# Kernel tuning notes

Measured on AMD Instinct MI355X. Metric: run time of the kernel, lower is better.

Reference implementation:

```python
import jax, jax.numpy as jnp
import numpy as np

IN_SIZE = 64
RES = 1024
B = 16
T = 2048
ALPHA = 0.5
SPECTRAL_RADIUS = 0.9


def setup_inputs() -> dict:
    key = jax.random.key(0)
    ks = jax.random.split(key, 8)
    # W_hh scaled so spectral radius ~ SPECTRAL_RADIUS (circular law: |eig|max ~ sqrt(R)*std)
    scale_hh = SPECTRAL_RADIUS / np.sqrt(RES)
    return {
        "x": jax.random.normal(ks[0], (B, T, IN_SIZE), dtype=jnp.float32),
        "W_in0": jax.random.normal(ks[1], (IN_SIZE, RES), dtype=jnp.float32) * 0.5,
        "W_hh0": jax.random.normal(ks[2], (RES, RES), dtype=jnp.float32) * scale_hh,
        "b0": jax.random.normal(ks[3], (1, RES), dtype=jnp.float32) * 0.5,
        "W_in1": jax.random.normal(ks[4], (RES, RES), dtype=jnp.float32) * 0.1,
        "W_hh1": jax.random.normal(ks[5], (RES, RES), dtype=jnp.float32) * scale_hh,
        "b1": jax.random.normal(ks[6], (1, RES), dtype=jnp.float32) * 0.5,
        "readout": jax.random.normal(ks[7], (2 * RES, IN_SIZE), dtype=jnp.float32) * 0.02,
    }


def _reservoir_layer(xs, W_in, W_hh, b, alpha):
    # xs: [T, B, F] time-major; sequential leaky-integrator scan over T
    h0 = jnp.zeros((xs.shape[1], W_hh.shape[0]), dtype=xs.dtype)

    def step(h, x_i):
        h = (1.0 - alpha) * h + alpha * jnp.tanh(x_i @ W_in + h @ W_hh + b)
        return h, h

    _, states = jax.lax.scan(step, h0, xs)
    return states  # [T, B, R]


def reference(x, W_in0, W_hh0, b0, W_in1, W_hh1, b1, readout):
    xt = jnp.transpose(x, (1, 0, 2))  # [T, B, in]
    s0 = _reservoir_layer(xt, W_in0, W_hh0, b0, ALPHA)  # [T, B, R]
    s1 = _reservoir_layer(s0, W_in1, W_hh1, b1, ALPHA)  # [T, B, R]
    h = jnp.concatenate([s0, s1], axis=-1)  # [T, B, 2R]
    out = h @ readout  # [T, B, in]
    return jnp.transpose(out, (1, 0, 2))  # [B, T, in]
```

## Files before the change

kernel.cpp:

```cpp
#include <hip/hip_runtime.h>
#include <math.h>

#define ESN_B 16
#define ESN_T 2048
#define ESN_R 1024
#define ESN_IN 64
#define NBR (ESN_B * ESN_R)

#define OFF_WT_HH0 0
#define OFF_WT_IN1 (1024 * 1024)
#define OFF_WT_HH1 (2 * 1024 * 1024)
#define OFF_WT_IN0 (3 * 1024 * 1024)
#define OFF_RT     (OFF_WT_IN0 + 1024 * 64)
#define OFF_S0G    (OFF_RT + 64 * 2048)
#define OFF_S1G    (OFF_S0G + 2 * NBR)
#define OFF_FLAGS  (OFF_S1G + 2 * NBR)

typedef float vfloat4 __attribute__((__vector_size__(16)));

__global__ void __launch_bounds__(256) transpose_k(const float* __restrict__ src,
                                                   float* __restrict__ dst,
                                                   int rows, int cols) {
  __shared__ float tile[32][33];
  int bx = blockIdx.x * 32, by = blockIdx.y * 32;
  int tx = threadIdx.x, ty = threadIdx.y;
  #pragma unroll
  for (int i = ty; i < 32; i += 8) {
    int r = by + i, c = bx + tx;
    if (r < rows && c < cols) tile[i][tx] = src[(size_t)r * cols + c];
  }
  __syncthreads();
  #pragma unroll
  for (int i = ty; i < 32; i += 8) {
    int c = bx + i, r = by + tx;
    if (c < cols && r < rows) dst[(size_t)c * rows + r] = tile[tx][i];
  }
}

__device__ __forceinline__ float fast_tanh(float v) {
  float a = fabsf(v);
  float e = __expf(-2.0f * a);
  float t = __fdividef(1.0f - e, 1.0f + e);
  return copysignf(t, v);
}

__device__ __forceinline__ float dot4(float4 a, float4 b, float acc) {
  acc = fmaf(a.x, b.x, acc);
  acc = fmaf(a.y, b.y, acc);
  acc = fmaf(a.z, b.z, acc);
  acc = fmaf(a.w, b.w, acc);
  return acc;
}

__device__ __forceinline__ float wave_red64(float v) {
  #pragma unroll
  for (int off = 32; off > 0; off >>= 1) v += __shfl_xor(v, off, 64);
  return v;
}

__device__ __forceinline__ float reduce2(float a0, float a1, bool lb0) {
  float u = lb0 ? a0 : a1, k = lb0 ? a1 : a0;
  float A = k + __shfl_xor(u, 1, 64);
  A += __shfl_xor(A, 2, 64);
  A += __shfl_xor(A, 4, 64);
  A += __shfl_xor(A, 8, 64);
  A += __shfl_xor(A, 16, 64);
  A += __shfl_xor(A, 32, 64);
  return A;
}

__device__ __forceinline__ void llc_store_f32x4(float* p, float4 v) {
  vfloat4 vv = {v.x, v.y, v.z, v.w};
  asm volatile("global_store_dwordx4 %0, %1, off sc1" :: "v"(p), "v"(vv) : "memory");
}
__device__ __forceinline__ void llc_store_u32(unsigned* p, unsigned v) {
  asm volatile("global_store_dword %0, %1, off sc1" :: "v"(p), "v"(v) : "memory");
}
__device__ __forceinline__ unsigned llc_load_u32(const unsigned* p) {
  unsigned f;
  asm volatile("global_load_dword %0, %1, off sc1\n\ts_waitcnt vmcnt(0)"
               : "=v"(f) : "v"(p) : "memory");
  return f;
}
__device__ __forceinline__ void vmcnt0() {
  asm volatile("s_waitcnt vmcnt(0)" ::: "memory");
}
__device__ __forceinline__ void barrier_only() {
  asm volatile("" ::: "memory");
  __builtin_amdgcn_s_barrier();
  asm volatile("" ::: "memory");
}
__device__ __forceinline__ void barrier_lgkm() {
  asm volatile("s_waitcnt lgkmcnt(0)" ::: "memory");
  __builtin_amdgcn_s_barrier();
  asm volatile("" ::: "memory");
}

__global__ void __launch_bounds__(512, 2) esn_scan_kernel(
    const float* __restrict__ x,
    const float* __restrict__ b0,
    const float* __restrict__ b1,
    float* __restrict__ wsf,
    float* __restrict__ out) {
  __shared__ float s0l[2][4][1024];
  __shared__ float s1l[4][1024];
  __shared__ __align__(16) float res[2][4][16];
  extern __shared__ float dyn_pad[];
  if (blockIdx.x == 0x7fffffffu) dyn_pad[0] = 1.0f;

  const float* wtHH0 = wsf + OFF_WT_HH0;
  const float* wtIN1 = wsf + OFF_WT_IN1;
  const float* wtHH1 = wsf + OFF_WT_HH1;
  const float* wtIN0 = wsf + OFF_WT_IN0;
  const float* rt    = wsf + OFF_RT;
  float* s0g = wsf + OFF_S0G;
  float* s1g = wsf + OFF_S1G;
  unsigned* flags = (unsigned*)(wsf + OFF_FLAGS);

  const int tid = threadIdx.x;
  const int l = tid & 63;
  const int w = tid >> 6;
  const int bid = blockIdx.x;
  const int g = bid >> 6;
  const int bg = bid & 63;
  const int batch0 = g * 4;
  const int wg = bg * 8 + w;
  const int c0 = wg * 2;
  const int wl2 = w * 2;
  const bool doRO = (w >= 4);
  const int rbl = w - 4;
  const int rb = batch0 + rbl;
  const int roc = bg;
  unsigned* gflags = flags + g * 64;
  const bool lb0 = (l & 1) != 0;

  float4 wA0_0, wA0_1, wA0_2, wA0_3, wA1_0, wA1_1, wA1_2, wA1_3;
  float4 wB0_0, wB0_1, wB0_2, wB0_3, wB1_0, wB1_1, wB1_2, wB1_3;
  float4 wC0_0, wC0_1, wC0_2, wC0_3, wC1_0, wC1_1, wC1_2, wC1_3;
  float4 rd0, rd1, rd2, rd3, rd4, rd5, rd6, rd7;

#define LOADW(cc) { \
    const float* pA = wtHH0 + (size_t)(c0 + cc) * ESN_R + l * 4; \
    const float* pB = wtIN1 + (size_t)(c0 + cc) * ESN_R + l * 4; \
    const float* pC = wtHH1 + (size_t)(c0 + cc) * ESN_R + l * 4; \
    wA##cc##_0 = *(const float4*)(pA);       wA##cc##_1 = *(const float4*)(pA + 256); \
    wA##cc##_2 = *(const float4*)(pA + 512); wA##cc##_3 = *(const float4*)(pA + 768); \
    wB##cc##_0 = *(const float4*)(pB);       wB##cc##_1 = *(const float4*)(pB + 256); \
    wB##cc##_2 = *(const float4*)(pB + 512); wB##cc##_3 = *(const float4*)(pB + 768); \
    wC##cc##_0 = *(const float4*)(pC);       wC##cc##_1 = *(const float4*)(pC + 256); \
    wC##cc##_2 = *(const float4*)(pC + 512); wC##cc##_3 = *(const float4*)(pC + 768); \
  }
  LOADW(0) LOADW(1)
#undef LOADW

  rd0 = rd1 = rd2 = rd3 = rd4 = rd5 = rd6 = rd7 = make_float4(0.f, 0.f, 0.f, 0.f);
  if (doRO) {
    const float* pr = rt + (size_t)roc * 2048 + l * 4;
    rd0 = *(const float4*)(pr);        rd1 = *(const float4*)(pr + 256);
    rd2 = *(const float4*)(pr + 512);  rd3 = *(const float4*)(pr + 768);
    rd4 = *(const float4*)(pr + 1024); rd5 = *(const float4*)(pr + 1280);
    rd6 = *(const float4*)(pr + 1536); rd7 = *(const float4*)(pr + 1792);
  }
  const float wI0 = wtIN0[(size_t)(c0 + 0) * ESN_IN + l];
  const float wI1 = wtIN0[(size_t)(c0 + 1) * ESN_IN + l];
  const float b0sel = b0[c0 + (l & 1)];
  const float b1sel = b1[c0 + (l & 1)];

  const float* sA0 = s0g + 0 * NBR + batch0 * ESN_R + tid * 4;
  const float* sA1 = s0g + 1 * NBR + batch0 * ESN_R + tid * 4;
  const float* sB0 = s1g + 0 * NBR + batch0 * ESN_R + tid * 4;
  const float* sB1 = s1g + 1 * NBR + batch0 * ESN_R + tid * 4;
  const int soff = (l >> 2) * ESN_R + (l & 3) * 4;
  float* st0A = s0g + 0 * NBR + batch0 * ESN_R + bg * 16 + soff;
  float* st0B = s0g + 1 * NBR + batch0 * ESN_R + bg * 16 + soff;
  float* st1A = s1g + 0 * NBR + batch0 * ESN_R + bg * 16 + soff;
  float* st1B = s1g + 1 * NBR + batch0 * ESN_R + bg * 16 + soff;
  const float* xbase = x + (size_t)batch0 * ESN_T * ESN_IN + l;

#define ESN_ROUND(SLOTC, rr)                                                   \
  {                                                                            \
    const bool doL0 = ((rr) < ESN_T);                                          \
    const bool doL1 = ((rr) >= 1 && (rr) <= ESN_T);                            \
    float xv0 = 0.f, xv1 = 0.f, xv2 = 0.f, xv3 = 0.f;                          \
    if (doL0) {                                                                \
      const float* xp = xbase + (size_t)(rr) * ESN_IN;                         \
      xv0 = xp[0 * ESN_T * ESN_IN];                                            \
      xv1 = xp[1 * ESN_T * ESN_IN];                                            \
      xv2 = xp[2 * ESN_T * ESN_IN];                                            \
      xv3 = xp[3 * ESN_T * ESN_IN];                                            \
    }                                                                          \
    vmcnt0();                                                                  \
    if ((rr) > 0) {                                                            \
      if (w == 0) {                                                            \
        while (!__all(llc_load_u32(&gflags[l]) >= (unsigned)(rr))) {}          \
      }                                                                        \
      barrier_only();                                               \
    }                                                                          \
    const float* p0 = SLOTC ? sA0 : sA1;        \
    const float* p1 = SLOTC ? sB0 : sB1;                                       \
    float4 t0, t1, u0, u1;                                                     \
    asm volatile(                                                              \
        "global_load_dwordx4 %0, %4, off sc1\n\t"                              \
        "global_load_dwordx4 %1, %5, off sc1\n\t"                              \
        "global_load_dwordx4 %2, %6, off sc1\n\t"                              \
        "global_load_dwordx4 %3, %7, off sc1\n\t"                              \
        "s_waitcnt vmcnt(2)"                                                   \
        : "=&v"(t0), "=&v"(t1), "=&v"(u0), "=&v"(u1)                           \
        : "v"(p0), "v"(p0 + 2048), "v"(p1), "v"(p1 + 2048)                     \
        : "memory");                                                           \
    {                                                                          \
      float* d0 = &s0l[SLOTC][0][0] + tid * 4;                                 \
      *(float4*)(d0)        = t0;                                              \
      *(float4*)(d0 + 2048) = t1;                                              \
    }                                                                          \
    barrier_lgkm();                  \
    if (doL0) {                                                                \
      _Pragma("unroll")                                                        \
      for (int bb = 0; bb < 4; ++bb) {                                         \
        const float* hp = &s0l[SLOTC][bb][l * 4];                              \
        float4 h0x = *(const float4*)(hp);                                     \
        float4 h1x = *(const float4*)(hp + 256);                               \
        float4 h2x = *(const float4*)(hp + 512);                               \
        float4 h3x = *(const float4*)(hp + 768);                               \
        float xb = (bb == 0) ? xv0 : (bb == 1) ? xv1 : (bb == 2) ? xv2 : xv3;  \
        float a0 = xb * wI0, a1 = xb * wI1;                                    \
        a0 = dot4(wA0_0, h0x, a0); a0 = dot4(wA0_1, h1x, a0);                  \
        a0 = dot4(wA0_2, h2x, a0); a0 = dot4(wA0_3, h3x, a0);                  \
        a1 = dot4(wA1_0, h0x, a1); a1 = dot4(wA1_1, h1x, a1);                  \
        a1 = dot4(wA1_2, h2x, a1); a1 = dot4(wA1_3, h3x, a1);                  \
        float C = reduce2(a0, a1, lb0);                                        \
        if (l < 2) {                                                           \
          float prev = s0l[SLOTC][bb][c0 + l];                                 \
          res[0][bb][wl2 + l] = 0.5f * prev + 0.5f * fast_tanh(C + b0sel);     \
        }                                                                      \
      }                                                                        \
    }                                                                          \
    vmcnt0();                                                                  \
    {                                                                          \
      float* d1 = &s1l[0][0] + tid * 4;                                        \
      *(float4*)(d1)        = u0;                                              \
      *(float4*)(d1 + 2048) = u1;                                              \
    }                                                                          \
    barrier_lgkm();                             \
    if (w == 0 && l < 16 && doL0) {                                            \
      float4 v0 = *(const float4*)&res[0][l >> 2][(l & 3) * 4];                \
      llc_store_f32x4(SLOTC ? st0B : st0A, v0);                                \
    }                                                                          \
    if (doL1) {                                                                \
      _Pragma("unroll")                                                        \
      for (int bb = 0; bb < 4; ++bb) {                                         \
        const float* hp = &s0l[SLOTC][bb][l * 4];                              \
        float4 h0x = *(const float4*)(hp);                                     \
        float4 h1x = *(const float4*)(hp + 256);                               \
        float4 h2x = *(const float4*)(hp + 512);                               \
        float4 h3x = *(const float4*)(hp + 768);                               \
        const float* gp = &s1l[bb][l * 4];                                     \
        float4 g0x = *(const float4*)(gp);                                     \
        float4 g1x = *(const float4*)(gp + 256);                               \
        float4 g2x = *(const float4*)(gp + 512);                               \
        float4 g3x = *(const float4*)(gp + 768);                               \
        float a0 = 0.f, a1 = 0.f;                                              \
        a0 = dot4(wB0_0, h0x, a0); a0 = dot4(wB0_1, h1x, a0);                  \
        a0 = dot4(wB0_2, h2x, a0); a0 = dot4(wB0_3, h3x, a0);                  \
        a0 = dot4(wC0_0, g0x, a0); a0 = dot4(wC0_1, g1x, a0);                  \
        a0 = dot4(wC0_2, g2x, a0); a0 = dot4(wC0_3, g3x, a0);                  \
        a1 = dot4(wB1_0, h0x, a1); a1 = dot4(wB1_1, h1x, a1);                  \
        a1 = dot4(wB1_2, h2x, a1); a1 = dot4(wB1_3, h3x, a1);                  \
        a1 = dot4(wC1_0, g0x, a1); a1 = dot4(wC1_1, g1x, a1);                  \
        a1 = dot4(wC1_2, g2x, a1); a1 = dot4(wC1_3, g3x, a1);                  \
        float C = reduce2(a0, a1, lb0);                                        \
        if (l < 2) {                                                           \
          float prev = s1l[bb][c0 + l];                                        \
          res[1][bb][wl2 + l] = 0.5f * prev + 0.5f * fast_tanh(C + b1sel);     \
        }                                                                      \
      }                                                                        \
    }                                                                          \
    barrier_lgkm();                                   \
    if (w == 0) {                                                              \
      if (l < 16 && doL1) {                                                    \
        float4 v1 = *(const float4*)&res[1][l >> 2][(l & 3) * 4];              \
        llc_store_f32x4(SLOTC ? st1B : st1A, v1);                              \
      }                                                                        \
      vmcnt0();                                                                \
      if (l == 0) llc_store_u32(&gflags[bg], (unsigned)((rr) + 1));            \
    }                                                                          \
    if ((rr) >= 2 && doRO) {                                                   \
      const float* sp = &s0l[1 - SLOTC][rbl][l * 4];                           \
      const float* tp = &s1l[rbl][l * 4];                                      \
      float a = 0.f;                                                           \
      a = dot4(rd0, *(const float4*)(sp), a);                                  \
      a = dot4(rd1, *(const float4*)(sp + 256), a);                            \
      a = dot4(rd2, *(const float4*)(sp + 512), a);                            \
      a = dot4(rd3, *(const float4*)(sp + 768), a);                            \
      a = dot4(rd4, *(const float4*)(tp), a);                                  \
      a = dot4(rd5, *(const float4*)(tp + 256), a);                            \
      a = dot4(rd6, *(const float4*)(tp + 512), a);                            \
      a = dot4(rd7, *(const float4*)(tp + 768), a);                            \
      a = wave_red64(a);                                                       \
      if (l == 0) out[((size_t)rb * ESN_T + ((rr) - 2)) * ESN_IN + roc] = a;   \
    }                                                                          \
  }

  for (int rp = 0; rp < (ESN_T + 2) / 2; ++rp) {
    const int r0 = rp * 2;
    ESN_ROUND(0, r0)
    ESN_ROUND(1, r0 + 1)
  }
#undef ESN_ROUND
}

extern "C" void kernel_launch(void* const* d_in, const int* in_sizes, int n_in,
                              void* d_out, int out_size, void* d_ws, size_t ws_size,
                              hipStream_t stream) {
  (void)in_sizes; (void)n_in; (void)out_size; (void)ws_size;
  const float* x     = (const float*)d_in[0];
  const float* w_in0 = (const float*)d_in[1];
  const float* w_hh0 = (const float*)d_in[2];
  const float* b0    = (const float*)d_in[3];
  const float* w_in1 = (const float*)d_in[4];
  const float* w_hh1 = (const float*)d_in[5];
  const float* b1    = (const float*)d_in[6];
  const float* rdo   = (const float*)d_in[7];
  float* out = (float*)d_out;
  float* wsf = (float*)d_ws;

  dim3 tb(32, 8);
  transpose_k<<<dim3(32, 32), tb, 0, stream>>>(w_hh0, wsf + OFF_WT_HH0, 1024, 1024);
  transpose_k<<<dim3(32, 32), tb, 0, stream>>>(w_in1, wsf + OFF_WT_IN1, 1024, 1024);
  transpose_k<<<dim3(32, 32), tb, 0, stream>>>(w_hh1, wsf + OFF_WT_HH1, 1024, 1024);
  transpose_k<<<dim3(32, 2),  tb, 0, stream>>>(w_in0, wsf + OFF_WT_IN0, 64, 1024);
  transpose_k<<<dim3(2, 64),  tb, 0, stream>>>(rdo,   wsf + OFF_RT, 2048, 64);

  (void)hipMemsetAsync(wsf + OFF_S0G + NBR, 0, NBR * sizeof(float), stream);
  (void)hipMemsetAsync(wsf + OFF_S1G, 0, NBR * sizeof(float), stream);
  (void)hipMemsetAsync(wsf + OFF_FLAGS, 0, 4 * 64 * sizeof(unsigned), stream);

  esn_scan_kernel<<<dim3(256), dim3(512), 40960, stream>>>(x, b0, b1, wsf, out);
}
```

Baseline: 12.17 ms.

## Use 1024-thread blocks with one output column per wave

Each block now runs 16 waves instead of 8, and each wave owns a single reservoir column rather than two. That halves per-thread weight registers and replaces the paired two-column reduction with a plain 64-lane reduction. Staging the shared state into LDS now takes one float4 per thread instead of two. The trade-off is larger workgroups with a 1-block-per-CU launch bound, and barriers that span more waves.

```diff
diff --git a/kernel.cpp b/kernel.cpp
--- a/kernel.cpp
+++ b/kernel.cpp
@@ -58,17 +58,6 @@
   return v;
 }
 
-__device__ __forceinline__ float reduce2(float a0, float a1, bool lb0) {
-  float u = lb0 ? a0 : a1, k = lb0 ? a1 : a0;
-  float A = k + __shfl_xor(u, 1, 64);
-  A += __shfl_xor(A, 2, 64);
-  A += __shfl_xor(A, 4, 64);
-  A += __shfl_xor(A, 8, 64);
-  A += __shfl_xor(A, 16, 64);
-  A += __shfl_xor(A, 32, 64);
-  return A;
-}
-
 __device__ __forceinline__ void llc_store_f32x4(float* p, float4 v) {
   vfloat4 vv = {v.x, v.y, v.z, v.w};
   asm volatile("global_store_dwordx4 %0, %1, off sc1" :: "v"(p), "v"(vv) : "memory");
@@ -96,7 +85,7 @@
   asm volatile("" ::: "memory");
 }
 
-__global__ void __launch_bounds__(512, 2) esn_scan_kernel(
+__global__ void __launch_bounds__(1024, 1) esn_scan_kernel(
     const float* __restrict__ x,
     const float* __restrict__ b0,
     const float* __restrict__ b1,
@@ -124,35 +113,28 @@
   const int g = bid >> 6;
   const int bg = bid & 63;
   const int batch0 = g * 4;
-  const int wg = bg * 8 + w;
-  const int c0 = wg * 2;
-  const int wl2 = w * 2;
-  const bool doRO = (w >= 4);
-  const int rbl = w - 4;
+  const int c0 = bg * 16 + w;
+  const bool doRO = (w >= 12);
+  const int rbl = w - 12;
   const int rb = batch0 + rbl;
   const int roc = bg;
   unsigned* gflags = flags + g * 64;
-  const bool lb0 = (l & 1) != 0;
-
-  float4 wA0_0, wA0_1, wA0_2, wA0_3, wA1_0, wA1_1, wA1_2, wA1_3;
-  float4 wB0_0, wB0_1, wB0_2, wB0_3, wB1_0, wB1_1, wB1_2, wB1_3;
-  float4 wC0_0, wC0_1, wC0_2, wC0_3, wC1_0, wC1_1, wC1_2, wC1_3;
+
+  float4 wA_0, wA_1, wA_2, wA_3;
+  float4 wB_0, wB_1, wB_2, wB_3;
+  float4 wC_0, wC_1, wC_2, wC_3;
   float4 rd0, rd1, rd2, rd3, rd4, rd5, rd6, rd7;
-
-#define LOADW(cc) { \
-    const float* pA = wtHH0 + (size_t)(c0 + cc) * ESN_R + l * 4; \
-    const float* pB = wtIN1 + (size_t)(c0 + cc) * ESN_R + l * 4; \
-    const float* pC = wtHH1 + (size_t)(c0 + cc) * ESN_R + l * 4; \
-    wA##cc##_0 = *(const float4*)(pA);       wA##cc##_1 = *(const float4*)(pA + 256); \
-    wA##cc##_2 = *(const float4*)(pA + 512); wA##cc##_3 = *(const float4*)(pA + 768); \
-    wB##cc##_0 = *(const float4*)(pB);       wB##cc##_1 = *(const float4*)(pB + 256); \
-    wB##cc##_2 = *(const float4*)(pB + 512); wB##cc##_3 = *(const float4*)(pB + 768); \
-    wC##cc##_0 = *(const float4*)(pC);       wC##cc##_1 = *(const float4*)(pC + 256); \
-    wC##cc##_2 = *(const float4*)(pC + 512); wC##cc##_3 = *(const float4*)(pC + 768); \
-  }
-  LOADW(0) LOADW(1)
-#undef LOADW
-
+  {
+    const float* pA = wtHH0 + (size_t)c0 * ESN_R + l * 4;
+    const float* pB = wtIN1 + (size_t)c0 * ESN_R + l * 4;
+    const float* pC = wtHH1 + (size_t)c0 * ESN_R + l * 4;
+    wA_0 = *(const float4*)(pA);       wA_1 = *(const float4*)(pA + 256);
+    wA_2 = *(const float4*)(pA + 512); wA_3 = *(const float4*)(pA + 768);
+    wB_0 = *(const float4*)(pB);       wB_1 = *(const float4*)(pB + 256);
+    wB_2 = *(const float4*)(pB + 512); wB_3 = *(const float4*)(pB + 768);
+    wC_0 = *(const float4*)(pC);       wC_1 = *(const float4*)(pC + 256);
+    wC_2 = *(const float4*)(pC + 512); wC_3 = *(const float4*)(pC + 768);
+  }
   rd0 = rd1 = rd2 = rd3 = rd4 = rd5 = rd6 = rd7 = make_float4(0.f, 0.f, 0.f, 0.f);
   if (doRO) {
     const float* pr = rt + (size_t)roc * 2048 + l * 4;
@@ -161,10 +143,9 @@
     rd4 = *(const float4*)(pr + 1024); rd5 = *(const float4*)(pr + 1280);
     rd6 = *(const float4*)(pr + 1536); rd7 = *(const float4*)(pr + 1792);
   }
-  const float wI0 = wtIN0[(size_t)(c0 + 0) * ESN_IN + l];
-  const float wI1 = wtIN0[(size_t)(c0 + 1) * ESN_IN + l];
-  const float b0sel = b0[c0 + (l & 1)];
-  const float b1sel = b1[c0 + (l & 1)];
+  const float wI = wtIN0[(size_t)c0 * ESN_IN + l];
+  const float b0sel = b0[c0];
+  const float b1sel = b1[c0];
 
   const float* sA0 = s0g + 0 * NBR + batch0 * ESN_R + tid * 4;
   const float* sA1 = s0g + 1 * NBR + batch0 * ESN_R + tid * 4;
@@ -198,22 +179,16 @@
     }                                                                          \
     const float* p0 = SLOTC ? sA0 : sA1;        \
     const float* p1 = SLOTC ? sB0 : sB1;                                       \
-    float4 t0, t1, u0, u1;                                                     \
+    float4 t0, u0;                                                             \
     asm volatile(                                                              \
-        "global_load_dwordx4 %0, %4, off sc1\n\t"                              \
-        "global_load_dwordx4 %1, %5, off sc1\n\t"                              \
-        "global_load_dwordx4 %2, %6, off sc1\n\t"                              \
-        "global_load_dwordx4 %3, %7, off sc1\n\t"                              \
-        "s_waitcnt vmcnt(2)"                                                   \
-        : "=&v"(t0), "=&v"(t1), "=&v"(u0), "=&v"(u1)                           \
-        : "v"(p0), "v"(p0 + 2048), "v"(p1), "v"(p1 + 2048)                     \
+        "global_load_dwordx4 %0, %2, off sc1\n\t"                              \
+        "global_load_dwordx4 %1, %3, off sc1\n\t"                              \
+        "s_waitcnt vmcnt(1)"                                                   \
+        : "=&v"(t0), "=&v"(u0)                                                 \
+        : "v"(p0), "v"(p1)                                                     \
         : "memory");                                                           \
-    {                                                                          \
-      float* d0 = &s0l[SLOTC][0][0] + tid * 4;                                 \
-      *(float4*)(d0)        = t0;                                              \
-      *(float4*)(d0 + 2048) = t1;                                              \
-    }                                                                          \
-    barrier_lgkm();                  \
+    *(float4*)(&s0l[SLOTC][0][0] + tid * 4) = t0;                              \
+    barrier_lgkm();                   \
     if (doL0) {                                                                \
       _Pragma("unroll")                                                        \
       for (int bb = 0; bb < 4; ++bb) {                                         \
@@ -223,24 +198,18 @@
         float4 h2x = *(const float4*)(hp + 512);                               \
         float4 h3x = *(const float4*)(hp + 768);                               \
         float xb = (bb == 0) ? xv0 : (bb == 1) ? xv1 : (bb == 2) ? xv2 : xv3;  \
-        float a0 = xb * wI0, a1 = xb * wI1;                                    \
-        a0 = dot4(wA0_0, h0x, a0); a0 = dot4(wA0_1, h1x, a0);                  \
-        a0 = dot4(wA0_2, h2x, a0); a0 = dot4(wA0_3, h3x, a0);                  \
-        a1 = dot4(wA1_0, h0x, a1); a1 = dot4(wA1_1, h1x, a1);                  \
-        a1 = dot4(wA1_2, h2x, a1); a1 = dot4(wA1_3, h3x, a1);                  \
-        float C = reduce2(a0, a1, lb0);                                        \
-        if (l < 2) {                                                           \
-          float prev = s0l[SLOTC][bb][c0 + l];                                 \
-          res[0][bb][wl2 + l] = 0.5f * prev + 0.5f * fast_tanh(C + b0sel);     \
+        float a0 = xb * wI;                                                    \
+        a0 = dot4(wA_0, h0x, a0); a0 = dot4(wA_1, h1x, a0);                    \
+        a0 = dot4(wA_2, h2x, a0); a0 = dot4(wA_3, h3x, a0);                    \
+        float C = wave_red64(a0);                                              \
+        if (l == 0) {                                                          \
+          float prev = s0l[SLOTC][bb][c0];                                     \
+          res[0][bb][w] = 0.5f * prev + 0.5f * fast_tanh(C + b0sel);           \
         }                                                                      \
       }                                                                        \
     }                                                                          \
     vmcnt0();                                                                  \
-    {                                                                          \
-      float* d1 = &s1l[0][0] + tid * 4;                                        \
-      *(float4*)(d1)        = u0;                                              \
-      *(float4*)(d1 + 2048) = u1;                                              \
-    }                                                                          \
+    *(float4*)(&s1l[0][0] + tid * 4) = u0;                                     \
     barrier_lgkm();                             \
     if (w == 0 && l < 16 && doL0) {                                            \
       float4 v0 = *(const float4*)&res[0][l >> 2][(l & 3) * 4];                \
@@ -259,19 +228,15 @@
         float4 g1x = *(const float4*)(gp + 256);                               \
         float4 g2x = *(const float4*)(gp + 512);                               \
         float4 g3x = *(const float4*)(gp + 768);                               \
-        float a0 = 0.f, a1 = 0.f;                                              \
-        a0 = dot4(wB0_0, h0x, a0); a0 = dot4(wB0_1, h1x, a0);                  \
-        a0 = dot4(wB0_2, h2x, a0); a0 = dot4(wB0_3, h3x, a0);                  \
-        a0 = dot4(wC0_0, g0x, a0); a0 = dot4(wC0_1, g1x, a0);                  \
-        a0 = dot4(wC0_2, g2x, a0); a0 = dot4(wC0_3, g3x, a0);                  \
-        a1 = dot4(wB1_0, h0x, a1); a1 = dot4(wB1_1, h1x, a1);                  \
-        a1 = dot4(wB1_2, h2x, a1); a1 = dot4(wB1_3, h3x, a1);                  \
-        a1 = dot4(wC1_0, g0x, a1); a1 = dot4(wC1_1, g1x, a1);                  \
-        a1 = dot4(wC1_2, g2x, a1); a1 = dot4(wC1_3, g3x, a1);                  \
-        float C = reduce2(a0, a1, lb0);                                        \
-        if (l < 2) {                                                           \
-          float prev = s1l[bb][c0 + l];                                        \
-          res[1][bb][wl2 + l] = 0.5f * prev + 0.5f * fast_tanh(C + b1sel);     \
+        float a0 = 0.f;                                                        \
+        a0 = dot4(wB_0, h0x, a0); a0 = dot4(wB_1, h1x, a0);                    \
+        a0 = dot4(wB_2, h2x, a0); a0 = dot4(wB_3, h3x, a0);                    \
+        a0 = dot4(wC_0, g0x, a0); a0 = dot4(wC_1, g1x, a0);                    \
+        a0 = dot4(wC_2, g2x, a0); a0 = dot4(wC_3, g3x, a0);                    \
+        float C = wave_red64(a0);                                              \
+        if (l == 0) {                                                          \
+          float prev = s1l[bb][c0];                                            \
+          res[1][bb][w] = 0.5f * prev + 0.5f * fast_tanh(C + b1sel);           \
         }                                                                      \
       }                                                                        \
     }                                                                          \
@@ -335,5 +300,5 @@
   (void)hipMemsetAsync(wsf + OFF_S1G, 0, NBR * sizeof(float), stream);
   (void)hipMemsetAsync(wsf + OFF_FLAGS, 0, 4 * 64 * sizeof(unsigned), stream);
 
-  esn_scan_kernel<<<dim3(256), dim3(512), 40960, stream>>>(x, b0, b1, wsf, out);
-}
+  esn_scan_kernel<<<dim3(256), dim3(1024), 40960, stream>>>(x, b0, b1, wsf, out);
+}
```

New measurement: 18.19 ms. 49.5% more time.

## Merge layer-0 and layer-1 round phases into one pass with joint reduction

Applied to the files above, without the earlier changes.

Fuses the separate layer-0 and layer-1 compute phases of each scan round into a single loop. All four accumulators are reduced in one combined cross-lane shuffle tree, and both layers' states are stored by one wave in a single store phase. This removes one workgroup barrier and one wait-for-memory point per round, shortening the serial critical path of the 2048-step scan. In exchange it waits on all global state loads before any compute, and it raises register pressure from holding more live accumulators and h/g vectors at once.

```diff
diff --git a/kernel.cpp b/kernel.cpp
--- a/kernel.cpp
+++ b/kernel.cpp
@@ -58,15 +58,19 @@
   return v;
 }
 
-__device__ __forceinline__ float reduce2(float a0, float a1, bool lb0) {
-  float u = lb0 ? a0 : a1, k = lb0 ? a1 : a0;
-  float A = k + __shfl_xor(u, 1, 64);
-  A += __shfl_xor(A, 2, 64);
-  A += __shfl_xor(A, 4, 64);
-  A += __shfl_xor(A, 8, 64);
-  A += __shfl_xor(A, 16, 64);
-  A += __shfl_xor(A, 32, 64);
-  return A;
+__device__ __forceinline__ float reduce4(float a0, float a1, float a2, float a3,
+                                         bool lb0, bool lb1) {
+  float uA = lb0 ? a0 : a1, kA = lb0 ? a1 : a0;
+  float A = kA + __shfl_xor(uA, 1, 64);
+  float uB = lb0 ? a2 : a3, kB = lb0 ? a3 : a2;
+  float B = kB + __shfl_xor(uB, 1, 64);
+  float uC = lb1 ? A : B, kC = lb1 ? B : A;
+  float C = kC + __shfl_xor(uC, 2, 64);
+  C += __shfl_xor(C, 4, 64);
+  C += __shfl_xor(C, 8, 64);
+  C += __shfl_xor(C, 16, 64);
+  C += __shfl_xor(C, 32, 64);
+  return C;
 }
 
 __device__ __forceinline__ void llc_store_f32x4(float* p, float4 v) {
@@ -133,6 +137,7 @@
   const int roc = bg;
   unsigned* gflags = flags + g * 64;
   const bool lb0 = (l & 1) != 0;
+  const bool lb1 = (l & 2) != 0;
 
   float4 wA0_0, wA0_1, wA0_2, wA0_3, wA1_0, wA1_1, wA1_2, wA1_3;
   float4 wB0_0, wB0_1, wB0_2, wB0_3, wB1_0, wB1_1, wB1_2, wB1_3;
@@ -163,18 +168,17 @@
   }
   const float wI0 = wtIN0[(size_t)(c0 + 0) * ESN_IN + l];
   const float wI1 = wtIN0[(size_t)(c0 + 1) * ESN_IN + l];
-  const float b0sel = b0[c0 + (l & 1)];
-  const float b1sel = b1[c0 + (l & 1)];
+  float bsel = 0.f;
+  if (l < 4) bsel = ((l < 2) ? b0 : b1)[c0 + (l & 1)];
 
   const float* sA0 = s0g + 0 * NBR + batch0 * ESN_R + tid * 4;
   const float* sA1 = s0g + 1 * NBR + batch0 * ESN_R + tid * 4;
   const float* sB0 = s1g + 0 * NBR + batch0 * ESN_R + tid * 4;
   const float* sB1 = s1g + 1 * NBR + batch0 * ESN_R + tid * 4;
-  const int soff = (l >> 2) * ESN_R + (l & 3) * 4;
-  float* st0A = s0g + 0 * NBR + batch0 * ESN_R + bg * 16 + soff;
-  float* st0B = s0g + 1 * NBR + batch0 * ESN_R + bg * 16 + soff;
-  float* st1A = s1g + 0 * NBR + batch0 * ESN_R + bg * 16 + soff;
-  float* st1B = s1g + 1 * NBR + batch0 * ESN_R + bg * 16 + soff;
+  float* gb = ((l < 16) ? s0g : s1g) +
+              (batch0 + ((l >> 2) & 3)) * ESN_R + bg * 16 + (l & 3) * 4;
+  float* gbA = gb;
+  float* gbB = gb + NBR;
   const float* xbase = x + (size_t)batch0 * ESN_T * ESN_IN + l;
 
 #define ESN_ROUND(SLOTC, rr)                                                   \
@@ -189,12 +193,11 @@
       xv2 = xp[2 * ESN_T * ESN_IN];                                            \
       xv3 = xp[3 * ESN_T * ESN_IN];                                            \
     }                                                                          \
-    vmcnt0();                                                                  \
     if ((rr) > 0) {                                                            \
       if (w == 0) {                                                            \
         while (!__all(llc_load_u32(&gflags[l]) >= (unsigned)(rr))) {}          \
       }                                                                        \
-      barrier_only();                                               \
+      barrier_only();            \
     }                                                                          \
     const float* p0 = SLOTC ? sA0 : sA1;        \
     const float* p1 = SLOTC ? sB0 : sB1;                                       \
@@ -204,82 +207,60 @@
         "global_load_dwordx4 %1, %5, off sc1\n\t"                              \
         "global_load_dwordx4 %2, %6, off sc1\n\t"                              \
         "global_load_dwordx4 %3, %7, off sc1\n\t"                              \
-        "s_waitcnt vmcnt(2)"                                                   \
+        "s_waitcnt vmcnt(0)"                                                   \
         : "=&v"(t0), "=&v"(t1), "=&v"(u0), "=&v"(u1)                           \
         : "v"(p0), "v"(p0 + 2048), "v"(p1), "v"(p1 + 2048)                     \
         : "memory");                                                           \
     {                                                                          \
       float* d0 = &s0l[SLOTC][0][0] + tid * 4;                                 \
+      float* d1 = &s1l[0][0] + tid * 4;                                        \
       *(float4*)(d0)        = t0;                                              \
       *(float4*)(d0 + 2048) = t1;                                              \
-    }                                                                          \
-    barrier_lgkm();                  \
-    if (doL0) {                                                                \
-      _Pragma("unroll")                                                        \
-      for (int bb = 0; bb < 4; ++bb) {                                         \
-        const float* hp = &s0l[SLOTC][bb][l * 4];                              \
-        float4 h0x = *(const float4*)(hp);                                     \
-        float4 h1x = *(const float4*)(hp + 256);                               \
-        float4 h2x = *(const float4*)(hp + 512);                               \
-        float4 h3x = *(const float4*)(hp + 768);                               \
-        float xb = (bb == 0) ? xv0 : (bb == 1) ? xv1 : (bb == 2) ? xv2 : xv3;  \
-        float a0 = xb * wI0, a1 = xb * wI1;                                    \
-        a0 = dot4(wA0_0, h0x, a0); a0 = dot4(wA0_1, h1x, a0);                  \
-        a0 = dot4(wA0_2, h2x, a0); a0 = dot4(wA0_3, h3x, a0);                  \
-        a1 = dot4(wA1_0, h0x, a1); a1 = dot4(wA1_1, h1x, a1);                  \
-        a1 = dot4(wA1_2, h2x, a1); a1 = dot4(wA1_3, h3x, a1);                  \
-        float C = reduce2(a0, a1, lb0);                                        \
-        if (l < 2) {                                                           \
-          float prev = s0l[SLOTC][bb][c0 + l];                                 \
-          res[0][bb][wl2 + l] = 0.5f * prev + 0.5f * fast_tanh(C + b0sel);     \
-        }                                                                      \
-      }                                                                        \
-    }                                                                          \
-    vmcnt0();                                                                  \
-    {                                                                          \
-      float* d1 = &s1l[0][0] + tid * 4;                                        \
       *(float4*)(d1)        = u0;                                              \
       *(float4*)(d1 + 2048) = u1;                                              \
     }                                                                          \
-    barrier_lgkm();                             \
-    if (w == 0 && l < 16 && doL0) {                                            \
-      float4 v0 = *(const float4*)&res[0][l >> 2][(l & 3) * 4];                \
-      llc_store_f32x4(SLOTC ? st0B : st0A, v0);                                \
-    }                                                                          \
-    if (doL1) {                                                                \
-      _Pragma("unroll")                                                        \
-      for (int bb = 0; bb < 4; ++bb) {                                         \
-        const float* hp = &s0l[SLOTC][bb][l * 4];                              \
-        float4 h0x = *(const float4*)(hp);                                     \
-        float4 h1x = *(const float4*)(hp + 256);                               \
-        float4 h2x = *(const float4*)(hp + 512);                               \
-        float4 h3x = *(const float4*)(hp + 768);                               \
-        const float* gp = &s1l[bb][l * 4];                                     \
-        float4 g0x = *(const float4*)(gp);                                     \
-        float4 g1x = *(const float4*)(gp + 256);                               \
-        float4 g2x = *(const float4*)(gp + 512);                               \
-        float4 g3x = *(const float4*)(gp + 768);                               \
-        float a0 = 0.f, a1 = 0.f;                                              \
-        a0 = dot4(wB0_0, h0x, a0); a0 = dot4(wB0_1, h1x, a0);                  \
-        a0 = dot4(wB0_2, h2x, a0); a0 = dot4(wB0_3, h3x, a0);                  \
-        a0 = dot4(wC0_0, g0x, a0); a0 = dot4(wC0_1, g1x, a0);                  \
-        a0 = dot4(wC0_2, g2x, a0); a0 = dot4(wC0_3, g3x, a0);                  \
-        a1 = dot4(wB1_0, h0x, a1); a1 = dot4(wB1_1, h1x, a1);                  \
-        a1 = dot4(wB1_2, h2x, a1); a1 = dot4(wB1_3, h3x, a1);                  \
-        a1 = dot4(wC1_0, g0x, a1); a1 = dot4(wC1_1, g1x, a1);                  \
-        a1 = dot4(wC1_2, g2x, a1); a1 = dot4(wC1_3, g3x, a1);                  \
-        float C = reduce2(a0, a1, lb0);                                        \
-        if (l < 2) {                                                           \
-          float prev = s1l[bb][c0 + l];                                        \
-          res[1][bb][wl2 + l] = 0.5f * prev + 0.5f * fast_tanh(C + b1sel);     \
-        }                                                                      \
+    barrier_lgkm();                                \
+    _Pragma("unroll")                                                          \
+    for (int bb = 0; bb < 4; ++bb) {                                           \
+      const float* hp = &s0l[SLOTC][bb][l * 4];                                \
+      float4 h0x = *(const float4*)(hp);                                       \
+      float4 h1x = *(const float4*)(hp + 256);                                 \
+      float4 h2x = *(const float4*)(hp + 512);                                 \
+      float4 h3x = *(const float4*)(hp + 768);                                 \
+      const float* gp = &s1l[bb][l * 4];                                       \
+      float4 g0x = *(const float4*)(gp);                                       \
+      float4 g1x = *(const float4*)(gp + 256);                                 \
+      float4 g2x = *(const float4*)(gp + 512);                                 \
+      float4 g3x = *(const float4*)(gp + 768);                                 \
+      float xb = (bb == 0) ? xv0 : (bb == 1) ? xv1 : (bb == 2) ? xv2 : xv3;    \
+      float a0 = xb * wI0, a1 = xb * wI1;                                      \
+      a0 = dot4(wA0_0, h0x, a0); a0 = dot4(wA0_1, h1x, a0);                    \
+      a0 = dot4(wA0_2, h2x, a0); a0 = dot4(wA0_3, h3x, a0);                    \
+      a1 = dot4(wA1_0, h0x, a1); a1 = dot4(wA1_1, h1x, a1);                    \
+      a1 = dot4(wA1_2, h2x, a1); a1 = dot4(wA1_3, h3x, a1);                    \
+      float a2 = 0.f, a3 = 0.f;                                                \
+      a2 = dot4(wB0_0, h0x, a2); a2 = dot4(wB0_1, h1x, a2);                    \
+      a2 = dot4(wB0_2, h2x, a2); a2 = dot4(wB0_3, h3x, a2);                    \
+      a2 = dot4(wC0_0, g0x, a2); a2 = dot4(wC0_1, g1x, a2);                    \
+      a2 = dot4(wC0_2, g2x, a2); a2 = dot4(wC0_3, g3x, a2);                    \
+      a3 = dot4(wB1_0, h0x, a3); a3 = dot4(wB1_1, h1x, a3);                    \
+      a3 = dot4(wB1_2, h2x, a3); a3 = dot4(wB1_3, h3x, a3);                    \
+      a3 = dot4(wC1_0, g0x, a3); a3 = dot4(wC1_1, g1x, a3);                    \
+      a3 = dot4(wC1_2, g2x, a3); a3 = dot4(wC1_3, g3x, a3);                    \
+      float C = reduce4(a0, a1, a2, a3, lb0, lb1);                             \
+      if (l < 4) {                 \
+        const float* pbase = (l < 2) ? &s0l[SLOTC][bb][0] : &s1l[bb][0];       \
+        float prev = pbase[c0 + (l & 1)];                                      \
+        float nv = 0.5f * prev + 0.5f * fast_tanh(C + bsel);                   \
+        bool wr = (l < 2) ? doL0 : doL1;                                       \
+        if (wr) res[l >> 1][bb][wl2 + (l & 1)] = nv;                           \
       }                                                                        \
     }                                                                          \
-    barrier_lgkm();                                   \
+    barrier_lgkm();                                      \
     if (w == 0) {                                                              \
-      if (l < 16 && doL1) {                                                    \
-        float4 v1 = *(const float4*)&res[1][l >> 2][(l & 3) * 4];              \
-        llc_store_f32x4(SLOTC ? st1B : st1A, v1);                              \
+      if (l < 32 && ((l < 16) ? doL0 : doL1)) {                                \
+        float4 v = *(const float4*)&res[l >> 4][(l >> 2) & 3][(l & 3) * 4];    \
+        llc_store_f32x4(SLOTC ? gbB : gbA, v);                                 \
       }                                                                        \
       vmcnt0();                                                                \
       if (l == 0) llc_store_u32(&gflags[bg], (unsigned)((rr) + 1));            \
@@ -332,7 +313,7 @@
   transpose_k<<<dim3(2, 64),  tb, 0, stream>>>(rdo,   wsf + OFF_RT, 2048, 64);
 
   (void)hipMemsetAsync(wsf + OFF_S0G + NBR, 0, NBR * sizeof(float), stream);
-  (void)hipMemsetAsync(wsf + OFF_S1G, 0, NBR * sizeof(float), stream);
+  (void)hipMemsetAsync(wsf + OFF_S1G, 0, 2 * NBR * sizeof(float), stream);
   (void)hipMemsetAsync(wsf + OFF_FLAGS, 0, 4 * 64 * sizeof(unsigned), stream);
 
   esn_scan_kernel<<<dim3(256), dim3(512), 40960, stream>>>(x, b0, b1, wsf, out);
```

Result: faster. 11.48 ms (-5.7%).
